# Performance work log

Hardware: AMD Instinct MI355X
Metric: run time of the kernel (lower is better)

## Reference

```python
import jax, jax.numpy as jnp
import numpy as np

N_ITERS = 10


def setup_inputs() -> dict:
    key = jax.random.key(0)
    x = jax.random.normal(key, (1, 4096, 8192), dtype=jnp.float32)
    return {"x": x}


def reference(x):
    # x: (1, d, n). Squeeze batch as in fun().
    a = x[0]  # (d, n)
    # sklearn MinMaxScaler(feature_range=(0,1)): per-column (feature) scaling
    data_min = jnp.min(a, axis=0)  # (n,)
    data_max = jnp.max(a, axis=0)  # (n,)
    data_range = data_max - data_min
    safe_range = jnp.where(data_range == 0, 1.0, data_range)  # sklearn's _handle_zeros_in_scale
    arr = (a - data_min) / safe_range  # fit_transform

    def step(arr, i):
        # p = row - mean(row); note abs(p)*sign(p) == p, kept as written for faithfulness
        p = arr - jnp.mean(arr, axis=1, keepdims=True)
        arr = arr * (1.0 - jnp.abs(p) * jnp.sign(p)) + jnp.where(i == 0, 0.001, 0.0)
        return arr, None

    arr, _ = jax.lax.scan(step, arr, jnp.arange(N_ITERS))
    # inverse_transform: X * safe_range + data_min (sklearn uses the zero-safe scale)
    out = arr * safe_range + data_min
    return out.reshape(1, -1, out.shape[-1])
```

## Files before the change

kernel.cpp:

```cpp
#include <hip/hip_runtime.h>

#define DROWS 4096
#define NCOLS 8192

__device__ __forceinline__ unsigned encf(float f) {
    unsigned u = __float_as_uint(f);
    return (u & 0x80000000u) ? ~u : (u | 0x80000000u);
}
__device__ __forceinline__ float decf(unsigned u) {
    unsigned v = (u & 0x80000000u) ? (u ^ 0x80000000u) : ~u;
    return __uint_as_float(v);
}

__global__ __launch_bounds__(256) void colminmax(const float* __restrict__ x,
                                                 unsigned* __restrict__ mine,
                                                 unsigned* __restrict__ maxe) {
    int c = blockIdx.x * 1024 + threadIdx.x * 4;
    int r0 = blockIdx.y * 64;
    const float* p = x + (size_t)r0 * NCOLS + c;

    float4 mn = *(const float4*)p;
    float4 mx = mn;
#pragma unroll 8
    for (int i = 1; i < 64; ++i) {
        float4 v = *(const float4*)(p + (size_t)i * NCOLS);
        mn.x = fminf(mn.x, v.x); mn.y = fminf(mn.y, v.y);
        mn.z = fminf(mn.z, v.z); mn.w = fminf(mn.w, v.w);
        mx.x = fmaxf(mx.x, v.x); mx.y = fmaxf(mx.y, v.y);
        mx.z = fmaxf(mx.z, v.z); mx.w = fmaxf(mx.w, v.w);
    }
    atomicMin(&mine[c + 0], encf(mn.x));
    atomicMin(&mine[c + 1], encf(mn.y));
    atomicMin(&mine[c + 2], encf(mn.z));
    atomicMin(&mine[c + 3], encf(mn.w));
    atomicMax(&maxe[c + 0], encf(mx.x));
    atomicMax(&maxe[c + 1], encf(mx.y));
    atomicMax(&maxe[c + 2], encf(mx.z));
    atomicMax(&maxe[c + 3], encf(mx.w));
}

__global__ __launch_bounds__(256) void finalize_minmax(unsigned* __restrict__ mine,
                                                       unsigned* __restrict__ maxe,
                                                       float* __restrict__ fmin) {
    int i = blockIdx.x * 256 + threadIdx.x;
    float mn = decf(mine[i]);
    float mx = decf(maxe[i]);
    float r = mx - mn;
    float sr = (r == 0.0f) ? 1.0f : r;
    fmin[i] = mn;
    ((float*)mine)[i] = sr;
    ((float*)maxe)[i] = 1.0f / sr;
}

__device__ __forceinline__ float block_sum(float v, float* red, int slot) {
#pragma unroll
    for (int m = 32; m; m >>= 1) v += __shfl_xor(v, m, 64);
    int wid = threadIdx.x >> 6;
    int lane = threadIdx.x & 63;
    if (lane == 0) red[slot * 4 + wid] = v;
    __syncthreads();
    float* r = red + slot * 4;
    return r[0] + r[1] + r[2] + r[3];
}

__global__ __launch_bounds__(256, 6) void rowiter(const float* __restrict__ x,
                                                  const float* __restrict__ fmin,
                                                  const float* __restrict__ fsr,
                                                  const float* __restrict__ finv,
                                                  float* __restrict__ out) {
    int row = blockIdx.x;
    int t = threadIdx.x;
    const float* xr = x + (size_t)row * NCOLS;
    float* outr = out + (size_t)row * NCOLS;

    __shared__ float red[8];

    float4 a[8];
    float psum = 0.0f;
#pragma unroll
    for (int k = 0; k < 8; ++k) {
        int c = k * 1024 + t * 4;
        float4 v = *(const float4*)(xr + c);
        float4 mn = *(const float4*)(fmin + c);
        float4 iv = *(const float4*)(finv + c);
        float4 u;
        u.x = (v.x - mn.x) * iv.x;
        u.y = (v.y - mn.y) * iv.y;
        u.z = (v.z - mn.z) * iv.z;
        u.w = (v.w - mn.w) * iv.w;
        a[k] = u;
        psum += (u.x + u.y) + (u.z + u.w);
    }
    float sum = block_sum(psum, red, 0);

#pragma unroll
    for (int it = 0; it < 10; ++it) {
        float mean = sum * (1.0f / 8192.0f);
        float add = (it == 0) ? 0.001f : 0.0f;
        psum = 0.0f;
#pragma unroll
        for (int k = 0; k < 8; ++k) {
            float4 u = a[k];
            u.x = u.x * (1.0f - (u.x - mean)) + add;
            u.y = u.y * (1.0f - (u.y - mean)) + add;
            u.z = u.z * (1.0f - (u.z - mean)) + add;
            u.w = u.w * (1.0f - (u.w - mean)) + add;
            a[k] = u;
            psum += (u.x + u.y) + (u.z + u.w);
        }
        if (it < 9) sum = block_sum(psum, red, (it + 1) & 1);
    }

#pragma unroll
    for (int k = 0; k < 8; ++k) {
        int c = k * 1024 + t * 4;
        float4 mn = *(const float4*)(fmin + c);
        float4 sr = *(const float4*)(fsr + c);
        float4 u = a[k];
        float* o = outr + c;
        __builtin_nontemporal_store(fmaf(u.x, sr.x, mn.x), o + 0);
        __builtin_nontemporal_store(fmaf(u.y, sr.y, mn.y), o + 1);
        __builtin_nontemporal_store(fmaf(u.z, sr.z, mn.z), o + 2);
        __builtin_nontemporal_store(fmaf(u.w, sr.w, mn.w), o + 3);
    }
}

extern "C" void kernel_launch(void* const* d_in, const int* in_sizes, int n_in,
                              void* d_out, int out_size, void* d_ws, size_t ws_size,
                              hipStream_t stream) {
    const float* x = (const float*)d_in[0];
    float* out = (float*)d_out;

    unsigned* mine = (unsigned*)d_ws;
    unsigned* maxe = mine + NCOLS;
    float* fmin = (float*)(maxe + NCOLS);

    hipMemsetAsync(mine, 0xFF, NCOLS * sizeof(unsigned), stream);
    hipMemsetAsync(maxe, 0x00, NCOLS * sizeof(unsigned), stream);
    colminmax<<<dim3(NCOLS / 1024, DROWS / 64), 256, 0, stream>>>(x, mine, maxe);
    finalize_minmax<<<NCOLS / 256, 256, 0, stream>>>(mine, maxe, fmin);
    rowiter<<<DROWS, 256, 0, stream>>>(x, fmin, (const float*)mine,
                                       (const float*)maxe, out);
}
```

Measured before the change: 88.24 us.

## Replace atomic column min/max with partial buffers and fold mean into FMA

Column min/max now writes per-tile partial results to a workspace buffer, and a second kernel reduces them. This removes the two memsets and the global atomics, and the old atomic path stays as a fallback when the workspace is too small. The row iteration is also rewritten as u*(1+mean-u)+add with an fmaf. The last iteration is peeled into the store loop so its unused block reduction is skipped. The cost is 4 MB of extra partial-buffer traffic and a serial 64-step reduction in the finalize kernel.

```diff
diff --git a/kernel.cpp b/kernel.cpp
--- a/kernel.cpp
+++ b/kernel.cpp
@@ -2,44 +2,85 @@
 
 #define DROWS 4096
 #define NCOLS 8192
-
-__device__ __forceinline__ unsigned encf(float f) {
-    unsigned u = __float_as_uint(f);
-    return (u & 0x80000000u) ? ~u : (u | 0x80000000u);
-}
-__device__ __forceinline__ float decf(unsigned u) {
-    unsigned v = (u & 0x80000000u) ? (u ^ 0x80000000u) : ~u;
-    return __uint_as_float(v);
-}
-
-__global__ __launch_bounds__(256) void colminmax(const float* __restrict__ x,
-                                                 unsigned* __restrict__ mine,
-                                                 unsigned* __restrict__ maxe) {
+#define RTILE 64
+#define NTILES (DROWS / RTILE)
+
+
+__global__ __launch_bounds__(256) void colminmax_part(const float* __restrict__ x,
+                                                      float* __restrict__ pmin,
+                                                      float* __restrict__ pmax) {
     int c = blockIdx.x * 1024 + threadIdx.x * 4;
-    int r0 = blockIdx.y * 64;
+    int r0 = blockIdx.y * RTILE;
     const float* p = x + (size_t)r0 * NCOLS + c;
 
     float4 mn = *(const float4*)p;
     float4 mx = mn;
 #pragma unroll 8
-    for (int i = 1; i < 64; ++i) {
+    for (int i = 1; i < RTILE; ++i) {
         float4 v = *(const float4*)(p + (size_t)i * NCOLS);
         mn.x = fminf(mn.x, v.x); mn.y = fminf(mn.y, v.y);
         mn.z = fminf(mn.z, v.z); mn.w = fminf(mn.w, v.w);
         mx.x = fmaxf(mx.x, v.x); mx.y = fmaxf(mx.y, v.y);
         mx.z = fmaxf(mx.z, v.z); mx.w = fmaxf(mx.w, v.w);
     }
-    atomicMin(&mine[c + 0], encf(mn.x));
-    atomicMin(&mine[c + 1], encf(mn.y));
-    atomicMin(&mine[c + 2], encf(mn.z));
-    atomicMin(&mine[c + 3], encf(mn.w));
-    atomicMax(&maxe[c + 0], encf(mx.x));
-    atomicMax(&maxe[c + 1], encf(mx.y));
-    atomicMax(&maxe[c + 2], encf(mx.z));
-    atomicMax(&maxe[c + 3], encf(mx.w));
-}
-
-__global__ __launch_bounds__(256) void finalize_minmax(unsigned* __restrict__ mine,
+    size_t o = (size_t)blockIdx.y * NCOLS + c;
+    *(float4*)(pmin + o) = mn;
+    *(float4*)(pmax + o) = mx;
+}
+
+__global__ __launch_bounds__(256) void finalize_part(const float* __restrict__ pmin,
+                                                     const float* __restrict__ pmax,
+                                                     float* __restrict__ fmin,
+                                                     float* __restrict__ fsr,
+                                                     float* __restrict__ finv) {
+    int col = blockIdx.x * 256 + threadIdx.x;
+    float mn = pmin[col];
+    float mx = pmax[col];
+#pragma unroll 9
+    for (int y = 1; y < NTILES; ++y) {
+        mn = fminf(mn, pmin[(size_t)y * NCOLS + col]);
+        mx = fmaxf(mx, pmax[(size_t)y * NCOLS + col]);
+    }
+    float r = mx - mn;
+    float sr = (r == 0.0f) ? 1.0f : r;
+    fmin[col] = mn;
+    fsr[col] = sr;
+    finv[col] = 1.0f / sr;
+}
+
+
+__device__ __forceinline__ unsigned encf(float f) {
+    unsigned u = __float_as_uint(f);
+    return (u & 0x80000000u) ? ~u : (u | 0x80000000u);
+}
+__device__ __forceinline__ float decf(unsigned u) {
+    unsigned v = (u & 0x80000000u) ? (u ^ 0x80000000u) : ~u;
+    return __uint_as_float(v);
+}
+
+__global__ __launch_bounds__(256) void colminmax_atomic(const float* __restrict__ x,
+                                                        unsigned* __restrict__ mine,
+                                                        unsigned* __restrict__ maxe) {
+    int c = blockIdx.x * 1024 + threadIdx.x * 4;
+    int r0 = blockIdx.y * RTILE;
+    const float* p = x + (size_t)r0 * NCOLS + c;
+    float4 mn = *(const float4*)p;
+    float4 mx = mn;
+#pragma unroll 8
+    for (int i = 1; i < RTILE; ++i) {
+        float4 v = *(const float4*)(p + (size_t)i * NCOLS);
+        mn.x = fminf(mn.x, v.x); mn.y = fminf(mn.y, v.y);
+        mn.z = fminf(mn.z, v.z); mn.w = fminf(mn.w, v.w);
+        mx.x = fmaxf(mx.x, v.x); mx.y = fmaxf(mx.y, v.y);
+        mx.z = fmaxf(mx.z, v.z); mx.w = fmaxf(mx.w, v.w);
+    }
+    atomicMin(&mine[c + 0], encf(mn.x)); atomicMin(&mine[c + 1], encf(mn.y));
+    atomicMin(&mine[c + 2], encf(mn.z)); atomicMin(&mine[c + 3], encf(mn.w));
+    atomicMax(&maxe[c + 0], encf(mx.x)); atomicMax(&maxe[c + 1], encf(mx.y));
+    atomicMax(&maxe[c + 2], encf(mx.z)); atomicMax(&maxe[c + 3], encf(mx.w));
+}
+
+__global__ __launch_bounds__(256) void finalize_atomic(unsigned* __restrict__ mine,
                                                        unsigned* __restrict__ maxe,
                                                        float* __restrict__ fmin) {
     int i = blockIdx.x * 256 + threadIdx.x;
@@ -51,6 +92,7 @@
     ((float*)mine)[i] = sr;
     ((float*)maxe)[i] = 1.0f / sr;
 }
+
 
 __device__ __forceinline__ float block_sum(float v, float* red, int slot) {
 #pragma unroll
@@ -94,34 +136,41 @@
     float sum = block_sum(psum, red, 0);
 
 #pragma unroll
-    for (int it = 0; it < 10; ++it) {
-        float mean = sum * (1.0f / 8192.0f);
+    for (int it = 0; it < 9; ++it) {
+        float c1 = 1.0f + sum * (1.0f / 8192.0f);
         float add = (it == 0) ? 0.001f : 0.0f;
         psum = 0.0f;
 #pragma unroll
         for (int k = 0; k < 8; ++k) {
             float4 u = a[k];
-            u.x = u.x * (1.0f - (u.x - mean)) + add;
-            u.y = u.y * (1.0f - (u.y - mean)) + add;
-            u.z = u.z * (1.0f - (u.z - mean)) + add;
-            u.w = u.w * (1.0f - (u.w - mean)) + add;
+            u.x = fmaf(u.x, c1 - u.x, add);
+            u.y = fmaf(u.y, c1 - u.y, add);
+            u.z = fmaf(u.z, c1 - u.z, add);
+            u.w = fmaf(u.w, c1 - u.w, add);
             a[k] = u;
             psum += (u.x + u.y) + (u.z + u.w);
         }
-        if (it < 9) sum = block_sum(psum, red, (it + 1) & 1);
-    }
-
-#pragma unroll
-    for (int k = 0; k < 8; ++k) {
-        int c = k * 1024 + t * 4;
-        float4 mn = *(const float4*)(fmin + c);
-        float4 sr = *(const float4*)(fsr + c);
-        float4 u = a[k];
-        float* o = outr + c;
-        __builtin_nontemporal_store(fmaf(u.x, sr.x, mn.x), o + 0);
-        __builtin_nontemporal_store(fmaf(u.y, sr.y, mn.y), o + 1);
-        __builtin_nontemporal_store(fmaf(u.z, sr.z, mn.z), o + 2);
-        __builtin_nontemporal_store(fmaf(u.w, sr.w, mn.w), o + 3);
+        sum = block_sum(psum, red, (it + 1) & 1);
+    }
+
+    {
+        float c1 = 1.0f + sum * (1.0f / 8192.0f);
+#pragma unroll
+        for (int k = 0; k < 8; ++k) {
+            int c = k * 1024 + t * 4;
+            float4 mn = *(const float4*)(fmin + c);
+            float4 sr = *(const float4*)(fsr + c);
+            float4 u = a[k];
+            u.x = u.x * (c1 - u.x);
+            u.y = u.y * (c1 - u.y);
+            u.z = u.z * (c1 - u.z);
+            u.w = u.w * (c1 - u.w);
+            float* o = outr + c;
+            __builtin_nontemporal_store(fmaf(u.x, sr.x, mn.x), o + 0);
+            __builtin_nontemporal_store(fmaf(u.y, sr.y, mn.y), o + 1);
+            __builtin_nontemporal_store(fmaf(u.z, sr.z, mn.z), o + 2);
+            __builtin_nontemporal_store(fmaf(u.w, sr.w, mn.w), o + 3);
+        }
     }
 }
 
@@ -131,14 +180,28 @@
     const float* x = (const float*)d_in[0];
     float* out = (float*)d_out;
 
-    unsigned* mine = (unsigned*)d_ws;
-    unsigned* maxe = mine + NCOLS;
-    float* fmin = (float*)(maxe + NCOLS);
-
-    hipMemsetAsync(mine, 0xFF, NCOLS * sizeof(unsigned), stream);
-    hipMemsetAsync(maxe, 0x00, NCOLS * sizeof(unsigned), stream);
-    colminmax<<<dim3(NCOLS / 1024, DROWS / 64), 256, 0, stream>>>(x, mine, maxe);
-    finalize_minmax<<<NCOLS / 256, 256, 0, stream>>>(mine, maxe, fmin);
-    rowiter<<<DROWS, 256, 0, stream>>>(x, fmin, (const float*)mine,
-                                       (const float*)maxe, out);
-}
+    size_t need = (size_t)NTILES * NCOLS * 2 * sizeof(float) + 3 * NCOLS * sizeof(float);
+
+    if (ws_size >= need) {
+        float* pmin = (float*)d_ws;
+        float* pmax = pmin + (size_t)NTILES * NCOLS;
+        float* fmin = pmax + (size_t)NTILES * NCOLS;
+        float* fsr = fmin + NCOLS;
+        float* finv = fsr + NCOLS;
+
+        colminmax_part<<<dim3(NCOLS / 1024, NTILES), 256, 0, stream>>>(x, pmin, pmax);
+        finalize_part<<<NCOLS / 256, 256, 0, stream>>>(pmin, pmax, fmin, fsr, finv);
+        rowiter<<<DROWS, 256, 0, stream>>>(x, fmin, fsr, finv, out);
+    } else {
+        unsigned* mine = (unsigned*)d_ws;
+        unsigned* maxe = mine + NCOLS;
+        float* fmin = (float*)(maxe + NCOLS);
+
+        hipMemsetAsync(mine, 0xFF, NCOLS * sizeof(unsigned), stream);
+        hipMemsetAsync(maxe, 0x00, NCOLS * sizeof(unsigned), stream);
+        colminmax_atomic<<<dim3(NCOLS / 1024, NTILES), 256, 0, stream>>>(x, mine, maxe);
+        finalize_atomic<<<NCOLS / 256, 256, 0, stream>>>(mine, maxe, fmin);
+        rowiter<<<DROWS, 256, 0, stream>>>(x, fmin, (const float*)mine,
+                                           (const float*)maxe, out);
+    }
+}
```

Result: faster. 74.47 us (-15.6%).
